# Performance work log

Measured on AMD Instinct MI355X. Metric: run time of the kernel, lower is better.

Reference implementation:

```python
import jax, jax.numpy as jnp
import numpy as np

B, S, D, H = 4, 2048, 1024, 16
HD = D // H

def rotate_half(x):
    x1, x2 = jnp.split(x, 2, axis=-1)
    return jnp.concatenate((-x2, x1), axis=-1)

def apply_rope(x, cos, sin):
    # x: [B,H,S,hd]; cos/sin: [S,hd] -> broadcast over B,H
    return x * cos[None, None] + rotate_half(x) * sin[None, None]

def setup_inputs() -> dict:
    key = jax.random.key(0)
    ks = jax.random.split(key, 8)
    x = jax.random.normal(ks[0], (B, S, D), dtype=jnp.float32)
    mask = jnp.triu(jnp.ones((S, S), dtype=bool), k=1)  # True = masked (causal)
    pos = jnp.arange(S, dtype=jnp.float32)[:, None]
    inv = 1.0 / (10000.0 ** (jnp.arange(0, HD, 2, dtype=jnp.float32) / HD))
    ang = pos * inv[None, :]  # [S, hd/2]
    ang = jnp.concatenate([ang, ang], axis=-1)  # [S, hd]
    rope_cos = jnp.cos(ang)
    rope_sin = jnp.sin(ang)
    scale = 1.0 / np.sqrt(D)
    Wq = jax.random.normal(ks[1], (D, D), dtype=jnp.float32) * scale
    Wk = jax.random.normal(ks[2], (D, D), dtype=jnp.float32) * scale
    Wv = jax.random.normal(ks[3], (D, D), dtype=jnp.float32) * scale
    Wo = jax.random.normal(ks[4], (D, D), dtype=jnp.float32) * scale
    z = jnp.zeros((D,), dtype=jnp.float32)
    return {"x": x, "mask": mask, "rope_cos": rope_cos, "rope_sin": rope_sin,
            "Wq": Wq, "bq": z, "Wk": Wk, "bk": z, "Wv": Wv, "bv": z, "Wo": Wo, "bo": z}

def reference(x, mask, rope_cos, rope_sin, Wq, bq, Wk, bk, Wv, bv, Wo, bo):
    b, s, d = x.shape
    def proj(W, bias):
        y = x @ W.T + bias  # torch Linear: x W^T + b
        return y.reshape(b, s, H, HD).transpose(0, 2, 1, 3)  # [B,H,S,hd]
    Q = apply_rope(proj(Wq, bq), rope_cos, rope_sin)
    K = apply_rope(proj(Wk, bk), rope_cos, rope_sin)
    V = proj(Wv, bv)
    scores = jnp.einsum('bhqd,bhkd->bhqk', Q, K) / jnp.sqrt(jnp.float32(HD))
    scores = jnp.where(mask[None, None], -jnp.inf, scores)
    attn = jax.nn.softmax(scores, axis=-1)
    ctx = jnp.einsum('bhqk,bhkd->bhqd', attn, V)
    ctx = ctx.transpose(0, 2, 1, 3).reshape(b, s, d)
    return ctx @ Wo.T + bo
```

## Files before the change

kernel.cpp:

```cpp
#include <hip/hip_runtime.h>
#include <hip/hip_bf16.h>

#define S_LEN 2048
#define D_MODEL 1024
#define NH 16
#define HDIM 64
#define B_SZ 4

typedef __attribute__((ext_vector_type(8))) short bf16x8;
typedef __attribute__((ext_vector_type(4))) float f32x4;

__device__ inline void gld16(const __hip_bfloat16* g, __hip_bfloat16* l) {
    __builtin_amdgcn_global_load_lds(
        (const __attribute__((address_space(1))) unsigned int*)g,
        (__attribute__((address_space(3))) unsigned int*)l, 16, 0, 0);
}

__device__ inline unsigned int pkbf(float a, float b) {
    float2 f; f.x = a; f.y = b;
    __hip_bfloat162 h = __float22bfloat162_rn(f);
    union { __hip_bfloat162 h; unsigned int u; } cv; cv.h = h; return cv.u;
}

__global__ __launch_bounds__(256) void f2bf4_kernel(const float4* __restrict__ in,
                                                    __hip_bfloat162* __restrict__ out,
                                                    int n4) {
    int i = blockIdx.x * 256 + threadIdx.x;
    if (i < n4) {
        float4 v = in[i];
        __hip_bfloat162 a, b;
        a.x = __float2bfloat16(v.x); a.y = __float2bfloat16(v.y);
        b.x = __float2bfloat16(v.z); b.y = __float2bfloat16(v.w);
        out[2 * i]     = a;
        out[2 * i + 1] = b;
    }
}

__global__ __launch_bounds__(256) void f2bfw_kernel(
    const float4* __restrict__ w0, const float4* __restrict__ w1,
    const float4* __restrict__ w2, const float4* __restrict__ w3,
    __hip_bfloat162* __restrict__ o0, __hip_bfloat162* __restrict__ o1,
    __hip_bfloat162* __restrict__ o2, __hip_bfloat162* __restrict__ o3) {
    const int z = blockIdx.y;
    const float4* in = (z == 0) ? w0 : (z == 1) ? w1 : (z == 2) ? w2 : w3;
    __hip_bfloat162* out = (z == 0) ? o0 : (z == 1) ? o1 : (z == 2) ? o2 : o3;
    int i = blockIdx.x * 256 + threadIdx.x;
    float4 v = in[i];
    __hip_bfloat162 a, b;
    a.x = __float2bfloat16(v.x); a.y = __float2bfloat16(v.y);
    b.x = __float2bfloat16(v.z); b.y = __float2bfloat16(v.w);
    out[2 * i]     = a;
    out[2 * i + 1] = b;
}

__device__ inline void gemm_mainloop(const __hip_bfloat16* __restrict__ X,
                                     const __hip_bfloat16* __restrict__ W,
                                     __hip_bfloat16* As, __hip_bfloat16* Bs,
                                     int m0, int n0, f32x4 acc[4][4]) {
    const int tid = threadIdx.x;
    const int wv = tid >> 6, lane = tid & 63, l15 = lane & 15, quad = lane >> 4;
    const int rw = (wv >> 1) * 64, cw = (wv & 1) * 64;
    const int r0 = tid >> 2, c0 = (tid & 3) * 8;
    const int r1 = (tid + 256) >> 2, c1 = ((tid + 256) & 3) * 8;
    const __hip_bfloat16* xa0 = &X[(size_t)(m0 + r0) * D_MODEL + c0];
    const __hip_bfloat16* xa1 = &X[(size_t)(m0 + r1) * D_MODEL + c1];
    const __hip_bfloat16* wa0 = &W[(size_t)(n0 + r0) * D_MODEL + c0];
    const __hip_bfloat16* wa1 = &W[(size_t)(n0 + r1) * D_MODEL + c1];
    const int la0 = r0 * 32 + c0, la1 = r1 * 32 + c1;

    gld16(xa0, &As[la0]); gld16(xa1, &As[la1]);
    gld16(wa0, &Bs[la0]); gld16(wa1, &Bs[la1]);
    __syncthreads();
    for (int k0 = 0; k0 < D_MODEL; k0 += 32) {
        const int buf = (k0 >> 5) & 1;
        if (k0 + 32 < D_MODEL) {
            const int o = (buf ^ 1) * 4096;
            gld16(xa0 + k0 + 32, &As[o + la0]);
            gld16(xa1 + k0 + 32, &As[o + la1]);
            gld16(wa0 + k0 + 32, &Bs[o + la0]);
            gld16(wa1 + k0 + 32, &Bs[o + la1]);
        }
        const __hip_bfloat16* Ab = &As[buf * 4096];
        const __hip_bfloat16* Bb = &Bs[buf * 4096];
        bf16x8 af[4], bfr[4];
#pragma unroll
        for (int t = 0; t < 4; t++)
            af[t] = *(const bf16x8*)&Ab[(rw + t * 16 + l15) * 32 + quad * 8];
#pragma unroll
        for (int t = 0; t < 4; t++)
            bfr[t] = *(const bf16x8*)&Bb[(cw + t * 16 + l15) * 32 + quad * 8];
#pragma unroll
        for (int mt = 0; mt < 4; mt++)
#pragma unroll
            for (int nt = 0; nt < 4; nt++)
                acc[mt][nt] = __builtin_amdgcn_mfma_f32_16x16x32_bf16(
                    af[mt], bfr[nt], acc[mt][nt], 0, 0, 0);
        __syncthreads();
    }
}

#define PT 136
__global__ __launch_bounds__(256) void qkv_kernel(
    const __hip_bfloat16* __restrict__ X,
    const __hip_bfloat16* __restrict__ W0, const __hip_bfloat16* __restrict__ W1,
    const __hip_bfloat16* __restrict__ W2,
    const float* __restrict__ b0, const float* __restrict__ b1,
    const float* __restrict__ b2,
    const float* __restrict__ rc, const float* __restrict__ rs,
    __hip_bfloat16* __restrict__ Qo, __hip_bfloat16* __restrict__ Ko,
    __hip_bfloat16* __restrict__ Vo) {
    __shared__ __hip_bfloat16 pool[16384];
    __hip_bfloat16* As = pool;
    __hip_bfloat16* Bs = pool + 8192;
    const int z = blockIdx.z;
    const __hip_bfloat16* W = (z == 0) ? W0 : ((z == 1) ? W1 : W2);
    const float* bias = (z == 0) ? b0 : ((z == 1) ? b1 : b2);
    f32x4 acc[4][4];
#pragma unroll
    for (int i = 0; i < 4; i++)
#pragma unroll
        for (int j = 0; j < 4; j++) acc[i][j] = (f32x4){0.f, 0.f, 0.f, 0.f};
    const int m0 = blockIdx.x * 128, n0 = blockIdx.y * 128;
    gemm_mainloop(X, W, As, Bs, m0, n0, acc);

    const int tid = threadIdx.x;
    const int wv = tid >> 6, lane = tid & 63, l15 = lane & 15, quad = lane >> 4;
    const int rw = (wv >> 1) * 64, cw = (wv & 1) * 64;

    if (z == 2) {
        __hip_bfloat16* T = pool;
        const int b = m0 >> 11, s0l = m0 & (S_LEN - 1);
#pragma unroll
        for (int hn = 0; hn < 2; hn++) {
            __syncthreads();
            if ((wv & 1) == hn) {
#pragma unroll
                for (int mt = 0; mt < 4; mt++)
#pragma unroll
                    for (int nt = 0; nt < 4; nt++)
#pragma unroll
                        for (int r = 0; r < 4; r++) {
                            int dl = nt * 16 + l15;
                            int ml = rw + mt * 16 + quad * 4 + r;
                            T[dl * PT + ml] =
                                __float2bfloat16(acc[mt][nt][r] + bias[n0 + hn * 64 + dl]);
                        }
            }
            __syncthreads();
            const int d = tid >> 2, sc = tid & 3;
            const int h = (n0 >> 6) + hn;
            size_t gb = ((size_t)((b * NH + h) * HDIM + d)) * S_LEN + s0l + sc * 32;
#pragma unroll
            for (int j = 0; j < 4; j++) {
                bf16x8 v = *(const bf16x8*)&T[d * PT + sc * 32 + j * 8];
                *(bf16x8*)&Vo[gb + j * 8] = v;
            }
        }
    } else {
        __hip_bfloat16* dst = (z == 0) ? Qo : Ko;
        const float qs = (z == 0) ? 0.18033688011112042f : 1.0f;
#pragma unroll
        for (int mt = 0; mt < 4; mt++)
#pragma unroll
            for (int r = 0; r < 4; r++) {
                int m = m0 + rw + mt * 16 + quad * 4 + r;
                int s = m & (S_LEN - 1), b = m >> 11;
#pragma unroll
                for (int nt = 0; nt < 2; nt++) {
                    int n1 = n0 + cw + nt * 16 + l15;
                    int h = n1 >> 6, hd1 = n1 & 63;
                    float y1 = acc[mt][nt][r] + bias[n1];
                    float y2 = acc[mt][nt + 2][r] + bias[n1 + 32];
                    float c1 = rc[s * HDIM + hd1], s1 = rs[s * HDIM + hd1];
                    float c2 = rc[s * HDIM + hd1 + 32], s2 = rs[s * HDIM + hd1 + 32];
                    size_t base = (((size_t)(b * NH + h)) * S_LEN + s) * HDIM;
                    dst[base + hd1]      = __float2bfloat16((y1 * c1 - y2 * s1) * qs);
                    dst[base + hd1 + 32] = __float2bfloat16((y2 * c2 + y1 * s2) * qs);
                }
            }
    }
}

#define SWZ(r, c) (((r) << 6) + ((c) ^ (((r) & 7) << 3)))
__global__ __launch_bounds__(256) void attn_kernel(
    const __hip_bfloat16* __restrict__ Q, const __hip_bfloat16* __restrict__ K,
    const __hip_bfloat16* __restrict__ VT, __hip_bfloat16* __restrict__ CTX) {
    __shared__ __hip_bfloat16 Kl[2][64 * 64];
    __shared__ __hip_bfloat16 Vl[2][64 * 64];
    __shared__ __hip_bfloat16 Pl[2][4][16 * 64];
    const int tid = threadIdx.x;
    const int wv = tid >> 6, lane = tid & 63, l15 = lane & 15, quad = lane >> 4;
    const int bh = blockIdx.x;
    const int pr = blockIdx.y;
    const int tA = pr, tC = 31 - pr;
    const int nkb = tC + 1;
    const size_t off = (size_t)bh * S_LEN * HDIM;
    const __hip_bfloat16* Qp = Q + off;
    const __hip_bfloat16* Kp = K + off;
    const __hip_bfloat16* Vp = VT + off;
    __hip_bfloat16* PC = &Pl[0][wv][0];
    __hip_bfloat16* PA = &Pl[1][wv][0];

    const int e0 = wv * 512 + lane * 8;
    const int r0 = e0 >> 6, c80 = e0 & 63;
    const int sw0 = c80 ^ ((r0 & 7) << 3);
    const int r1 = r0 + 32;
    const int sw1 = c80 ^ ((r1 & 7) << 3);
    const __hip_bfloat16* ks0 = Kp + r0 * 64 + sw0;
    const __hip_bfloat16* ks1 = Kp + r1 * 64 + sw1;
    const __hip_bfloat16* vs0 = Vp + (size_t)r0 * S_LEN + sw0;
    const __hip_bfloat16* vs1 = Vp + (size_t)r1 * S_LEN + sw1;

    auto stage = [&](int kb, int bsel) {
        const int ko = kb * 64;
        gld16(ks0 + (size_t)ko * 64, &Kl[bsel][e0]);
        gld16(ks1 + (size_t)ko * 64, &Kl[bsel][e0 + 2048]);
        gld16(vs0 + ko, &Vl[bsel][e0]);
        gld16(vs1 + ko, &Vl[bsel][e0 + 2048]);
    };

    bf16x8 qfA[2], qfC[2];
#pragma unroll
    for (int c = 0; c < 2; c++) {
        qfA[c] = *(const bf16x8*)&Qp[(size_t)(tA * 64 + wv * 16 + l15) * HDIM + c * 32 + quad * 8];
        qfC[c] = *(const bf16x8*)&Qp[(size_t)(tC * 64 + wv * 16 + l15) * HDIM + c * 32 + quad * 8];
    }

    float lA = 0.f, lC = 0.f;
    f32x4 accA[4], accC[4];
#pragma unroll
    for (int nt = 0; nt < 4; nt++) {
        accA[nt] = (f32x4){0.f, 0.f, 0.f, 0.f};
        accC[nt] = (f32x4){0.f, 0.f, 0.f, 0.f};
    }

    const int qrel = wv * 16 + l15;

    stage(0, 0);
    __syncthreads();
    for (int kb = 0; kb < nkb; kb++) {
        const int buf = kb & 1;
        if (kb + 1 < nkb) stage(kb + 1, buf ^ 1);
        const __hip_bfloat16* Kb_ = &Kl[buf][0];
        const __hip_bfloat16* Vb_ = &Vl[buf][0];

        const bool aAct = (kb <= tA);
        unsigned int pkC[8], pkA[8];

        f32x4 saC[4], saA[4];
#pragma unroll
        for (int st = 0; st < 4; st++) {
            saC[st] = (f32x4){0.f, 0.f, 0.f, 0.f};
            saA[st] = (f32x4){0.f, 0.f, 0.f, 0.f};
        }
        if (aAct) {
#pragma unroll
            for (int c = 0; c < 2; c++)
#pragma unroll
                for (int st = 0; st < 4; st++) {
                    bf16x8 kf = *(const bf16x8*)&Kb_[SWZ(st * 16 + l15, c * 32 + quad * 8)];
                    saC[st] = __builtin_amdgcn_mfma_f32_16x16x32_bf16(kf, qfC[c], saC[st], 0, 0, 0);
                    saA[st] = __builtin_amdgcn_mfma_f32_16x16x32_bf16(kf, qfA[c], saA[st], 0, 0, 0);
                }
        } else {
#pragma unroll
            for (int c = 0; c < 2; c++)
#pragma unroll
                for (int st = 0; st < 4; st++) {
                    bf16x8 kf = *(const bf16x8*)&Kb_[SWZ(st * 16 + l15, c * 32 + quad * 8)];
                    saC[st] = __builtin_amdgcn_mfma_f32_16x16x32_bf16(kf, qfC[c], saC[st], 0, 0, 0);
                }
        }

        {
            float ls = 0.f;
            if (kb == tC) {
#pragma unroll
                for (int st = 0; st < 4; st++) {
                    float p[4];
#pragma unroll
                    for (int r = 0; r < 4; r++) {
                        bool msk = (st * 16 + quad * 4 + r > qrel);
                        p[r] = msk ? 0.f : __builtin_exp2f(saC[st][r]);
                        ls += p[r];
                    }
                    pkC[st * 2 + 0] = pkbf(p[0], p[1]);
                    pkC[st * 2 + 1] = pkbf(p[2], p[3]);
                }
            } else {
#pragma unroll
                for (int st = 0; st < 4; st++) {
                    float p[4];
#pragma unroll
                    for (int r = 0; r < 4; r++) {
                        p[r] = __builtin_exp2f(saC[st][r]);
                        ls += p[r];
                    }
                    pkC[st * 2 + 0] = pkbf(p[0], p[1]);
                    pkC[st * 2 + 1] = pkbf(p[2], p[3]);
                }
            }
            ls += __shfl_xor(ls, 16);
            ls += __shfl_xor(ls, 32);
            lC += ls;
#pragma unroll
            for (int st = 0; st < 4; st++) {
                uint2 w; w.x = pkC[st * 2]; w.y = pkC[st * 2 + 1];
                *(uint2*)&PC[SWZ(l15, st * 16 + quad * 4)] = w;
            }
        }
        if (aAct) {
            float ls = 0.f;
            if (kb == tA) {
#pragma unroll
                for (int st = 0; st < 4; st++) {
                    float p[4];
#pragma unroll
                    for (int r = 0; r < 4; r++) {
                        bool msk = (st * 16 + quad * 4 + r > qrel);
                        p[r] = msk ? 0.f : __builtin_exp2f(saA[st][r]);
                        ls += p[r];
                    }
                    pkA[st * 2 + 0] = pkbf(p[0], p[1]);
                    pkA[st * 2 + 1] = pkbf(p[2], p[3]);
                }
            } else {
#pragma unroll
                for (int st = 0; st < 4; st++) {
                    float p[4];
#pragma unroll
                    for (int r = 0; r < 4; r++) {
                        p[r] = __builtin_exp2f(saA[st][r]);
                        ls += p[r];
                    }
                    pkA[st * 2 + 0] = pkbf(p[0], p[1]);
                    pkA[st * 2 + 1] = pkbf(p[2], p[3]);
                }
            }
            ls += __shfl_xor(ls, 16);
            ls += __shfl_xor(ls, 32);
            lA += ls;
#pragma unroll
            for (int st = 0; st < 4; st++) {
                uint2 w; w.x = pkA[st * 2]; w.y = pkA[st * 2 + 1];
                *(uint2*)&PA[SWZ(l15, st * 16 + quad * 4)] = w;
            }
        }

#pragma unroll
        for (int c = 0; c < 2; c++) {
            bf16x8 vf[4];
#pragma unroll
            for (int nt = 0; nt < 4; nt++)
                vf[nt] = *(const bf16x8*)&Vb_[SWZ(nt * 16 + l15, c * 32 + quad * 8)];
            {
                bf16x8 pf = *(const bf16x8*)&PC[SWZ(l15, c * 32 + quad * 8)];
#pragma unroll
                for (int nt = 0; nt < 4; nt++)
                    accC[nt] = __builtin_amdgcn_mfma_f32_16x16x32_bf16(vf[nt], pf, accC[nt], 0, 0, 0);
            }
            if (aAct) {
                bf16x8 pf = *(const bf16x8*)&PA[SWZ(l15, c * 32 + quad * 8)];
#pragma unroll
                for (int nt = 0; nt < 4; nt++)
                    accA[nt] = __builtin_amdgcn_mfma_f32_16x16x32_bf16(vf[nt], pf, accA[nt], 0, 0, 0);
            }
        }

        __syncthreads();
    }

    const int b = bh >> 4, h = bh & 15;
    {
        const int q = tA * 64 + wv * 16 + l15;
        const float inv = 1.0f / lA;
#pragma unroll
        for (int nt = 0; nt < 4; nt++) {
            uint2 st2;
            st2.x = pkbf(accA[nt][0] * inv, accA[nt][1] * inv);
            st2.y = pkbf(accA[nt][2] * inv, accA[nt][3] * inv);
            *(uint2*)&CTX[((size_t)(b * S_LEN + q)) * D_MODEL + h * HDIM + nt * 16 + quad * 4] = st2;
        }
    }
    {
        const int q = tC * 64 + wv * 16 + l15;
        const float inv = 1.0f / lC;
#pragma unroll
        for (int nt = 0; nt < 4; nt++) {
            uint2 st2;
            st2.x = pkbf(accC[nt][0] * inv, accC[nt][1] * inv);
            st2.y = pkbf(accC[nt][2] * inv, accC[nt][3] * inv);
            *(uint2*)&CTX[((size_t)(b * S_LEN + q)) * D_MODEL + h * HDIM + nt * 16 + quad * 4] = st2;
        }
    }
}

__global__ __launch_bounds__(256) void outproj_kernel(
    const __hip_bfloat16* __restrict__ X, const __hip_bfloat16* __restrict__ W,
    const float* __restrict__ bias, float* __restrict__ OUT) {
    __shared__ __hip_bfloat16 As[2 * 4096];
    __shared__ __hip_bfloat16 Bs[2 * 4096];
    f32x4 acc[4][4];
#pragma unroll
    for (int i = 0; i < 4; i++)
#pragma unroll
        for (int j = 0; j < 4; j++) acc[i][j] = (f32x4){0.f, 0.f, 0.f, 0.f};
    const int m0 = blockIdx.x * 128, n0 = blockIdx.y * 128;
    gemm_mainloop(X, W, As, Bs, m0, n0, acc);
    const int tid = threadIdx.x;
    const int wv = tid >> 6, lane = tid & 63, l15 = lane & 15, quad = lane >> 4;
    const int rw = (wv >> 1) * 64, cw = (wv & 1) * 64;
#pragma unroll
    for (int mt = 0; mt < 4; mt++)
#pragma unroll
        for (int r = 0; r < 4; r++) {
            int m = m0 + rw + mt * 16 + quad * 4 + r;
#pragma unroll
            for (int nt = 0; nt < 4; nt++) {
                int n = n0 + cw + nt * 16 + l15;
                OUT[(size_t)m * D_MODEL + n] = acc[mt][nt][r] + bias[n];
            }
        }
}

extern "C" void kernel_launch(void* const* d_in, const int* in_sizes, int n_in,
                              void* d_out, int out_size, void* d_ws, size_t ws_size,
                              hipStream_t stream) {
    const float* x  = (const float*)d_in[0];
    const float* rc = (const float*)d_in[2];
    const float* rs = (const float*)d_in[3];
    const float* Wq = (const float*)d_in[4];
    const float* bq = (const float*)d_in[5];
    const float* Wk = (const float*)d_in[6];
    const float* bk = (const float*)d_in[7];
    const float* Wv = (const float*)d_in[8];
    const float* bv = (const float*)d_in[9];
    const float* Wo = (const float*)d_in[10];
    const float* bo = (const float*)d_in[11];

    char* ws = (char*)d_ws;
    __hip_bfloat16* xbf = (__hip_bfloat16*)(ws);
    __hip_bfloat16* wqb = (__hip_bfloat16*)(ws + (16u << 20));
    __hip_bfloat16* wkb = (__hip_bfloat16*)(ws + (18u << 20));
    __hip_bfloat16* wvb = (__hip_bfloat16*)(ws + (20u << 20));
    __hip_bfloat16* wob = (__hip_bfloat16*)(ws + (22u << 20));
    __hip_bfloat16* Qb  = (__hip_bfloat16*)(ws + (24u << 20));
    __hip_bfloat16* Kb  = (__hip_bfloat16*)(ws + (40u << 20));
    __hip_bfloat16* Vb  = (__hip_bfloat16*)(ws + (56u << 20));
    __hip_bfloat16* Cb  = (__hip_bfloat16*)(ws + (72u << 20));
    float* out = (float*)d_out;

    f2bf4_kernel<<<8192, 256, 0, stream>>>((const float4*)x, (__hip_bfloat162*)xbf, 2097152);
    f2bfw_kernel<<<dim3(1024, 4), 256, 0, stream>>>(
        (const float4*)Wq, (const float4*)Wk, (const float4*)Wv, (const float4*)Wo,
        (__hip_bfloat162*)wqb, (__hip_bfloat162*)wkb, (__hip_bfloat162*)wvb,
        (__hip_bfloat162*)wob);

    qkv_kernel<<<dim3(64, 8, 3), 256, 0, stream>>>(xbf, wqb, wkb, wvb, bq, bk, bv,
                                                   rc, rs, Qb, Kb, Vb);
    attn_kernel<<<dim3(64, 16), 256, 0, stream>>>(Qb, Kb, Vb, Cb);
    outproj_kernel<<<dim3(64, 8), 256, 0, stream>>>(Cb, wob, bo, out);
}
```

Measured before the change: 302.6 us.

## Fuse Q and K projections in one block sharing the X tile

The QKV kernel now has two z-slices. One computes Q and K together, loading each X tile once and running MFMAs against both Wq and Wk tiles with two accumulator sets. The other computes V alone. This removes the redundant X loads for the K projection, at the cost of double the accumulator registers and more LDS per block, which may lower occupancy despite the launch_bounds hint. The load address setup is also simplified and the B-buffer stride is templated.

New measurement: 310.9 us. +2.7%, slower.

```diff
diff --git a/kernel.cpp b/kernel.cpp
--- a/kernel.cpp
+++ b/kernel.cpp
@@ -53,6 +53,7 @@
     out[2 * i + 1] = b;
 }
 
+template <int BSTRIDE>
 __device__ inline void gemm_mainloop(const __hip_bfloat16* __restrict__ X,
                                      const __hip_bfloat16* __restrict__ W,
                                      __hip_bfloat16* As, __hip_bfloat16* Bs,
@@ -61,12 +62,11 @@
     const int wv = tid >> 6, lane = tid & 63, l15 = lane & 15, quad = lane >> 4;
     const int rw = (wv >> 1) * 64, cw = (wv & 1) * 64;
     const int r0 = tid >> 2, c0 = (tid & 3) * 8;
-    const int r1 = (tid + 256) >> 2, c1 = ((tid + 256) & 3) * 8;
     const __hip_bfloat16* xa0 = &X[(size_t)(m0 + r0) * D_MODEL + c0];
-    const __hip_bfloat16* xa1 = &X[(size_t)(m0 + r1) * D_MODEL + c1];
+    const __hip_bfloat16* xa1 = xa0 + (size_t)64 * D_MODEL;
     const __hip_bfloat16* wa0 = &W[(size_t)(n0 + r0) * D_MODEL + c0];
-    const __hip_bfloat16* wa1 = &W[(size_t)(n0 + r1) * D_MODEL + c1];
-    const int la0 = r0 * 32 + c0, la1 = r1 * 32 + c1;
+    const __hip_bfloat16* wa1 = wa0 + (size_t)64 * D_MODEL;
+    const int la0 = r0 * 32 + c0, la1 = la0 + 2048;
 
     gld16(xa0, &As[la0]); gld16(xa1, &As[la1]);
     gld16(wa0, &Bs[la0]); gld16(wa1, &Bs[la1]);
@@ -74,14 +74,13 @@
     for (int k0 = 0; k0 < D_MODEL; k0 += 32) {
         const int buf = (k0 >> 5) & 1;
         if (k0 + 32 < D_MODEL) {
-            const int o = (buf ^ 1) * 4096;
-            gld16(xa0 + k0 + 32, &As[o + la0]);
-            gld16(xa1 + k0 + 32, &As[o + la1]);
-            gld16(wa0 + k0 + 32, &Bs[o + la0]);
-            gld16(wa1 + k0 + 32, &Bs[o + la1]);
+            gld16(xa0 + k0 + 32, &As[(buf ^ 1) * 4096 + la0]);
+            gld16(xa1 + k0 + 32, &As[(buf ^ 1) * 4096 + la1]);
+            gld16(wa0 + k0 + 32, &Bs[(buf ^ 1) * BSTRIDE + la0]);
+            gld16(wa1 + k0 + 32, &Bs[(buf ^ 1) * BSTRIDE + la1]);
         }
         const __hip_bfloat16* Ab = &As[buf * 4096];
-        const __hip_bfloat16* Bb = &Bs[buf * 4096];
+        const __hip_bfloat16* Bb = &Bs[buf * BSTRIDE];
         bf16x8 af[4], bfr[4];
 #pragma unroll
         for (int t = 0; t < 4; t++)
@@ -100,7 +99,7 @@
 }
 
 #define PT 136
-__global__ __launch_bounds__(256) void qkv_kernel(
+__global__ __launch_bounds__(256, 2) void qkv_kernel(
     const __hip_bfloat16* __restrict__ X,
     const __hip_bfloat16* __restrict__ W0, const __hip_bfloat16* __restrict__ W1,
     const __hip_bfloat16* __restrict__ W2,
@@ -109,26 +108,22 @@
     const float* __restrict__ rc, const float* __restrict__ rs,
     __hip_bfloat16* __restrict__ Qo, __hip_bfloat16* __restrict__ Ko,
     __hip_bfloat16* __restrict__ Vo) {
-    __shared__ __hip_bfloat16 pool[16384];
-    __hip_bfloat16* As = pool;
-    __hip_bfloat16* Bs = pool + 8192;
-    const int z = blockIdx.z;
-    const __hip_bfloat16* W = (z == 0) ? W0 : ((z == 1) ? W1 : W2);
-    const float* bias = (z == 0) ? b0 : ((z == 1) ? b1 : b2);
-    f32x4 acc[4][4];
-#pragma unroll
-    for (int i = 0; i < 4; i++)
-#pragma unroll
-        for (int j = 0; j < 4; j++) acc[i][j] = (f32x4){0.f, 0.f, 0.f, 0.f};
-    const int m0 = blockIdx.x * 128, n0 = blockIdx.y * 128;
-    gemm_mainloop(X, W, As, Bs, m0, n0, acc);
-
+    __shared__ __hip_bfloat16 As[2 * 4096];
+    __shared__ __hip_bfloat16 Bs[2 * 2 * 4096];
     const int tid = threadIdx.x;
     const int wv = tid >> 6, lane = tid & 63, l15 = lane & 15, quad = lane >> 4;
     const int rw = (wv >> 1) * 64, cw = (wv & 1) * 64;
-
-    if (z == 2) {
-        __hip_bfloat16* T = pool;
+    const int m0 = blockIdx.x * 128, n0 = blockIdx.y * 128;
+
+    if (blockIdx.z == 1) {
+        f32x4 acc[4][4];
+#pragma unroll
+        for (int i = 0; i < 4; i++)
+#pragma unroll
+            for (int j = 0; j < 4; j++) acc[i][j] = (f32x4){0.f, 0.f, 0.f, 0.f};
+        gemm_mainloop<8192>(X, W2, As, Bs, m0, n0, acc);
+
+        __hip_bfloat16* T = Bs;
         const int b = m0 >> 11, s0l = m0 & (S_LEN - 1);
 #pragma unroll
         for (int hn = 0; hn < 2; hn++) {
@@ -143,7 +138,7 @@
                             int dl = nt * 16 + l15;
                             int ml = rw + mt * 16 + quad * 4 + r;
                             T[dl * PT + ml] =
-                                __float2bfloat16(acc[mt][nt][r] + bias[n0 + hn * 64 + dl]);
+                                __float2bfloat16(acc[mt][nt][r] + b2[n0 + hn * 64 + dl]);
                         }
             }
             __syncthreads();
@@ -156,9 +151,73 @@
                 *(bf16x8*)&Vo[gb + j * 8] = v;
             }
         }
-    } else {
-        __hip_bfloat16* dst = (z == 0) ? Qo : Ko;
-        const float qs = (z == 0) ? 0.18033688011112042f : 1.0f;
+        return;
+    }
+
+    f32x4 acc0[4][4], acc1[4][4];
+#pragma unroll
+    for (int i = 0; i < 4; i++)
+#pragma unroll
+        for (int j = 0; j < 4; j++) {
+            acc0[i][j] = (f32x4){0.f, 0.f, 0.f, 0.f};
+            acc1[i][j] = (f32x4){0.f, 0.f, 0.f, 0.f};
+        }
+    {
+        const int r0 = tid >> 2, c0 = (tid & 3) * 8;
+        const __hip_bfloat16* xa0 = &X[(size_t)(m0 + r0) * D_MODEL + c0];
+        const __hip_bfloat16* xa1 = xa0 + (size_t)64 * D_MODEL;
+        const __hip_bfloat16* wq0 = &W0[(size_t)(n0 + r0) * D_MODEL + c0];
+        const __hip_bfloat16* wq1 = wq0 + (size_t)64 * D_MODEL;
+        const __hip_bfloat16* wk0 = &W1[(size_t)(n0 + r0) * D_MODEL + c0];
+        const __hip_bfloat16* wk1 = wk0 + (size_t)64 * D_MODEL;
+        const int la0 = r0 * 32 + c0, la1 = la0 + 2048;
+
+        gld16(xa0, &As[la0]);        gld16(xa1, &As[la1]);
+        gld16(wq0, &Bs[la0]);        gld16(wq1, &Bs[la1]);
+        gld16(wk0, &Bs[4096 + la0]); gld16(wk1, &Bs[4096 + la1]);
+        __syncthreads();
+        for (int k0 = 0; k0 < D_MODEL; k0 += 32) {
+            const int buf = (k0 >> 5) & 1;
+            if (k0 + 32 < D_MODEL) {
+                const int o = (buf ^ 1) * 4096, ob = (buf ^ 1) * 8192;
+                gld16(xa0 + k0 + 32, &As[o + la0]);
+                gld16(xa1 + k0 + 32, &As[o + la1]);
+                gld16(wq0 + k0 + 32, &Bs[ob + la0]);
+                gld16(wq1 + k0 + 32, &Bs[ob + la1]);
+                gld16(wk0 + k0 + 32, &Bs[ob + 4096 + la0]);
+                gld16(wk1 + k0 + 32, &Bs[ob + 4096 + la1]);
+            }
+            const __hip_bfloat16* Ab  = &As[buf * 4096];
+            const __hip_bfloat16* Bq  = &Bs[buf * 8192];
+            const __hip_bfloat16* Bk  = &Bs[buf * 8192 + 4096];
+            bf16x8 af[4], bq[4], bk[4];
+#pragma unroll
+            for (int t = 0; t < 4; t++)
+                af[t] = *(const bf16x8*)&Ab[(rw + t * 16 + l15) * 32 + quad * 8];
+#pragma unroll
+            for (int t = 0; t < 4; t++)
+                bq[t] = *(const bf16x8*)&Bq[(cw + t * 16 + l15) * 32 + quad * 8];
+#pragma unroll
+            for (int t = 0; t < 4; t++)
+                bk[t] = *(const bf16x8*)&Bk[(cw + t * 16 + l15) * 32 + quad * 8];
+#pragma unroll
+            for (int mt = 0; mt < 4; mt++)
+#pragma unroll
+                for (int nt = 0; nt < 4; nt++)
+                    acc0[mt][nt] = __builtin_amdgcn_mfma_f32_16x16x32_bf16(
+                        af[mt], bq[nt], acc0[mt][nt], 0, 0, 0);
+#pragma unroll
+            for (int mt = 0; mt < 4; mt++)
+#pragma unroll
+                for (int nt = 0; nt < 4; nt++)
+                    acc1[mt][nt] = __builtin_amdgcn_mfma_f32_16x16x32_bf16(
+                        af[mt], bk[nt], acc1[mt][nt], 0, 0, 0);
+            __syncthreads();
+        }
+    }
+
+    {
+        const float qs = 0.18033688011112042f;
 #pragma unroll
         for (int mt = 0; mt < 4; mt++)
 #pragma unroll
@@ -169,13 +228,34 @@
                 for (int nt = 0; nt < 2; nt++) {
                     int n1 = n0 + cw + nt * 16 + l15;
                     int h = n1 >> 6, hd1 = n1 & 63;
-                    float y1 = acc[mt][nt][r] + bias[n1];
-                    float y2 = acc[mt][nt + 2][r] + bias[n1 + 32];
+                    float y1 = acc0[mt][nt][r] + b0[n1];
+                    float y2 = acc0[mt][nt + 2][r] + b0[n1 + 32];
                     float c1 = rc[s * HDIM + hd1], s1 = rs[s * HDIM + hd1];
                     float c2 = rc[s * HDIM + hd1 + 32], s2 = rs[s * HDIM + hd1 + 32];
                     size_t base = (((size_t)(b * NH + h)) * S_LEN + s) * HDIM;
-                    dst[base + hd1]      = __float2bfloat16((y1 * c1 - y2 * s1) * qs);
-                    dst[base + hd1 + 32] = __float2bfloat16((y2 * c2 + y1 * s2) * qs);
+                    Qo[base + hd1]      = __float2bfloat16((y1 * c1 - y2 * s1) * qs);
+                    Qo[base + hd1 + 32] = __float2bfloat16((y2 * c2 + y1 * s2) * qs);
+                }
+            }
+    }
+    {
+#pragma unroll
+        for (int mt = 0; mt < 4; mt++)
+#pragma unroll
+            for (int r = 0; r < 4; r++) {
+                int m = m0 + rw + mt * 16 + quad * 4 + r;
+                int s = m & (S_LEN - 1), b = m >> 11;
+#pragma unroll
+                for (int nt = 0; nt < 2; nt++) {
+                    int n1 = n0 + cw + nt * 16 + l15;
+                    int h = n1 >> 6, hd1 = n1 & 63;
+                    float y1 = acc1[mt][nt][r] + b1[n1];
+                    float y2 = acc1[mt][nt + 2][r] + b1[n1 + 32];
+                    float c1 = rc[s * HDIM + hd1], s1 = rs[s * HDIM + hd1];
+                    float c2 = rc[s * HDIM + hd1 + 32], s2 = rs[s * HDIM + hd1 + 32];
+                    size_t base = (((size_t)(b * NH + h)) * S_LEN + s) * HDIM;
+                    Ko[base + hd1]      = __float2bfloat16(y1 * c1 - y2 * s1);
+                    Ko[base + hd1 + 32] = __float2bfloat16(y2 * c2 + y1 * s2);
                 }
             }
     }
@@ -406,7 +486,7 @@
 #pragma unroll
         for (int j = 0; j < 4; j++) acc[i][j] = (f32x4){0.f, 0.f, 0.f, 0.f};
     const int m0 = blockIdx.x * 128, n0 = blockIdx.y * 128;
-    gemm_mainloop(X, W, As, Bs, m0, n0, acc);
+    gemm_mainloop<4096>(X, W, As, Bs, m0, n0, acc);
     const int tid = threadIdx.x;
     const int wv = tid >> 6, lane = tid & 63, l15 = lane & 15, quad = lane >> 4;
     const int rw = (wv >> 1) * 64, cw = (wv & 1) * 64;
@@ -456,7 +536,7 @@
         (__hip_bfloat162*)wqb, (__hip_bfloat162*)wkb, (__hip_bfloat162*)wvb,
         (__hip_bfloat162*)wob);
 
-    qkv_kernel<<<dim3(64, 8, 3), 256, 0, stream>>>(xbf, wqb, wkb, wvb, bq, bk, bv,
+    qkv_kernel<<<dim3(64, 8, 2), 256, 0, stream>>>(xbf, wqb, wkb, wvb, bq, bk, bv,
                                                    rc, rs, Qb, Kb, Vb);
     attn_kernel<<<dim3(64, 16), 256, 0, stream>>>(Qb, Kb, Vb, Cb);
     outproj_kernel<<<dim3(64, 8), 256, 0, stream>>>(Cb, wob, bo, out);
```

## Use 256x256 tiles with 512 threads and swizzled LDS for QKV GEMM

Applied to the files above, without the earlier changes.

Replaces the 128x128, 256-thread QKV projection GEMM with a 256x256 tile computed by 8 waves, each holding an 8x4 MFMA accumulator block. K steps grow to 64 and the LDS staging uses an XOR swizzle to avoid bank conflicts. The aim is more operand reuse per loaded byte and fewer global loads. The trade-off is far fewer blocks (384 instead of 1536), which may underfill the GPU's CUs, plus higher register and LDS use per block.

New measurement: 328.2 us. 1.08x slower.

```diff
diff --git a/kernel.cpp b/kernel.cpp
--- a/kernel.cpp
+++ b/kernel.cpp
@@ -53,6 +53,143 @@
     out[2 * i + 1] = b;
 }
 
+__device__ inline void gemm256_mainloop(const __hip_bfloat16* __restrict__ X,
+                                        const __hip_bfloat16* __restrict__ W,
+                                        __hip_bfloat16* As, __hip_bfloat16* Bs,
+                                        int m0, int n0, f32x4 acc[8][4]) {
+    const int tid = threadIdx.x;
+    const int wv = tid >> 6, lane = tid & 63, l15 = lane & 15, quad = lane >> 4;
+    const int wr = wv >> 2, wc = wv & 3;
+    const int row_s = tid >> 3;
+    const int csw = ((tid & 7) ^ (row_s & 7)) * 8;
+    const __hip_bfloat16* xsrc = X + (size_t)(m0 + row_s) * D_MODEL + csw;
+    const __hip_bfloat16* wsrc = W + (size_t)(n0 + row_s) * D_MODEL + csw;
+    const int ld = tid * 8;
+
+    auto stage = [&](int k0, int bsel) {
+#pragma unroll
+        for (int i = 0; i < 4; i++) {
+            gld16(xsrc + (size_t)(i * 64) * D_MODEL + k0,
+                  &As[bsel * 16384 + i * 4096 + ld]);
+            gld16(wsrc + (size_t)(i * 64) * D_MODEL + k0,
+                  &Bs[bsel * 16384 + i * 4096 + ld]);
+        }
+    };
+
+    stage(0, 0);
+    __syncthreads();
+    for (int kt = 0; kt < 16; kt++) {
+        const int buf = kt & 1;
+        if (kt + 1 < 16) stage((kt + 1) * 64, buf ^ 1);
+        const __hip_bfloat16* Ab = &As[buf * 16384];
+        const __hip_bfloat16* Bb = &Bs[buf * 16384];
+#pragma unroll
+        for (int kc = 0; kc < 2; kc++) {
+            bf16x8 af[8], bfr[4];
+#pragma unroll
+            for (int mt = 0; mt < 8; mt++) {
+                int row = wr * 128 + mt * 16 + l15;
+                af[mt] = *(const bf16x8*)&Ab[row * 64 + (((kc * 4 + quad) ^ (l15 & 7)) * 8)];
+            }
+#pragma unroll
+            for (int nt = 0; nt < 4; nt++) {
+                int row = wc * 64 + nt * 16 + l15;
+                bfr[nt] = *(const bf16x8*)&Bb[row * 64 + (((kc * 4 + quad) ^ (l15 & 7)) * 8)];
+            }
+#pragma unroll
+            for (int mt = 0; mt < 8; mt++)
+#pragma unroll
+                for (int nt = 0; nt < 4; nt++)
+                    acc[mt][nt] = __builtin_amdgcn_mfma_f32_16x16x32_bf16(
+                        af[mt], bfr[nt], acc[mt][nt], 0, 0, 0);
+        }
+        __syncthreads();
+    }
+}
+
+#define PT 264
+__global__ __launch_bounds__(512, 2) void qkv_kernel(
+    const __hip_bfloat16* __restrict__ X,
+    const __hip_bfloat16* __restrict__ W0, const __hip_bfloat16* __restrict__ W1,
+    const __hip_bfloat16* __restrict__ W2,
+    const float* __restrict__ b0, const float* __restrict__ b1,
+    const float* __restrict__ b2,
+    const float* __restrict__ rc, const float* __restrict__ rs,
+    __hip_bfloat16* __restrict__ Qo, __hip_bfloat16* __restrict__ Ko,
+    __hip_bfloat16* __restrict__ Vo) {
+    __shared__ __hip_bfloat16 As[2 * 16384];
+    __shared__ __hip_bfloat16 Bs[2 * 16384];
+    const int z = blockIdx.z;
+    const __hip_bfloat16* W = (z == 0) ? W0 : ((z == 1) ? W1 : W2);
+    f32x4 acc[8][4];
+#pragma unroll
+    for (int i = 0; i < 8; i++)
+#pragma unroll
+        for (int j = 0; j < 4; j++) acc[i][j] = (f32x4){0.f, 0.f, 0.f, 0.f};
+    const int m0 = blockIdx.x * 256, n0 = blockIdx.y * 256;
+    gemm256_mainloop(X, W, As, Bs, m0, n0, acc);
+
+    const int tid = threadIdx.x;
+    const int wv = tid >> 6, lane = tid & 63, l15 = lane & 15, quad = lane >> 4;
+    const int wr = wv >> 2, wc = wv & 3;
+
+    if (z == 2) {
+        __hip_bfloat16* T = As;
+        const int b = m0 >> 11, s0l = m0 & (S_LEN - 1);
+#pragma unroll
+        for (int hn = 0; hn < 4; hn++) {
+            __syncthreads();
+            if (wc == hn) {
+#pragma unroll
+                for (int mt = 0; mt < 8; mt++)
+#pragma unroll
+                    for (int nt = 0; nt < 4; nt++)
+#pragma unroll
+                        for (int r = 0; r < 4; r++) {
+                            int dl = nt * 16 + l15;
+                            int ml = wr * 128 + mt * 16 + quad * 4 + r;
+                            T[dl * PT + ml] =
+                                __float2bfloat16(acc[mt][nt][r] + b2[n0 + hn * 64 + dl]);
+                        }
+            }
+            __syncthreads();
+            const int d = tid >> 3, sc = tid & 7;
+            const int h = (n0 >> 6) + hn;
+            size_t gb = ((size_t)((b * NH + h) * HDIM + d)) * S_LEN + s0l + sc * 32;
+#pragma unroll
+            for (int j = 0; j < 4; j++) {
+                bf16x8 v = *(const bf16x8*)&T[d * PT + sc * 32 + j * 8];
+                *(bf16x8*)&Vo[gb + j * 8] = v;
+            }
+        }
+        return;
+    }
+
+    __hip_bfloat16* dst = (z == 0) ? Qo : Ko;
+    const float* bias = (z == 0) ? b0 : b1;
+    const float qs = (z == 0) ? 0.18033688011112042f : 1.0f;
+#pragma unroll
+    for (int mt = 0; mt < 8; mt++)
+#pragma unroll
+        for (int r = 0; r < 4; r++) {
+            int m = m0 + wr * 128 + mt * 16 + quad * 4 + r;
+            int s = m & (S_LEN - 1), b = m >> 11;
+#pragma unroll
+            for (int nt = 0; nt < 2; nt++) {
+                int hd1 = nt * 16 + l15;
+                int n1 = n0 + wc * 64 + hd1;
+                int h = n1 >> 6;
+                float y1 = acc[mt][nt][r] + bias[n1];
+                float y2 = acc[mt][nt + 2][r] + bias[n1 + 32];
+                float c1 = rc[s * HDIM + hd1], s1 = rs[s * HDIM + hd1];
+                float c2 = rc[s * HDIM + hd1 + 32], s2 = rs[s * HDIM + hd1 + 32];
+                size_t base = (((size_t)(b * NH + h)) * S_LEN + s) * HDIM;
+                dst[base + hd1]      = __float2bfloat16((y1 * c1 - y2 * s1) * qs);
+                dst[base + hd1 + 32] = __float2bfloat16((y2 * c2 + y1 * s2) * qs);
+            }
+        }
+}
+
 __device__ inline void gemm_mainloop(const __hip_bfloat16* __restrict__ X,
                                      const __hip_bfloat16* __restrict__ W,
                                      __hip_bfloat16* As, __hip_bfloat16* Bs,
@@ -96,88 +233,6 @@
                 acc[mt][nt] = __builtin_amdgcn_mfma_f32_16x16x32_bf16(
                     af[mt], bfr[nt], acc[mt][nt], 0, 0, 0);
         __syncthreads();
-    }
-}
-
-#define PT 136
-__global__ __launch_bounds__(256) void qkv_kernel(
-    const __hip_bfloat16* __restrict__ X,
-    const __hip_bfloat16* __restrict__ W0, const __hip_bfloat16* __restrict__ W1,
-    const __hip_bfloat16* __restrict__ W2,
-    const float* __restrict__ b0, const float* __restrict__ b1,
-    const float* __restrict__ b2,
-    const float* __restrict__ rc, const float* __restrict__ rs,
-    __hip_bfloat16* __restrict__ Qo, __hip_bfloat16* __restrict__ Ko,
-    __hip_bfloat16* __restrict__ Vo) {
-    __shared__ __hip_bfloat16 pool[16384];
-    __hip_bfloat16* As = pool;
-    __hip_bfloat16* Bs = pool + 8192;
-    const int z = blockIdx.z;
-    const __hip_bfloat16* W = (z == 0) ? W0 : ((z == 1) ? W1 : W2);
-    const float* bias = (z == 0) ? b0 : ((z == 1) ? b1 : b2);
-    f32x4 acc[4][4];
-#pragma unroll
-    for (int i = 0; i < 4; i++)
-#pragma unroll
-        for (int j = 0; j < 4; j++) acc[i][j] = (f32x4){0.f, 0.f, 0.f, 0.f};
-    const int m0 = blockIdx.x * 128, n0 = blockIdx.y * 128;
-    gemm_mainloop(X, W, As, Bs, m0, n0, acc);
-
-    const int tid = threadIdx.x;
-    const int wv = tid >> 6, lane = tid & 63, l15 = lane & 15, quad = lane >> 4;
-    const int rw = (wv >> 1) * 64, cw = (wv & 1) * 64;
-
-    if (z == 2) {
-        __hip_bfloat16* T = pool;
-        const int b = m0 >> 11, s0l = m0 & (S_LEN - 1);
-#pragma unroll
-        for (int hn = 0; hn < 2; hn++) {
-            __syncthreads();
-            if ((wv & 1) == hn) {
-#pragma unroll
-                for (int mt = 0; mt < 4; mt++)
-#pragma unroll
-                    for (int nt = 0; nt < 4; nt++)
-#pragma unroll
-                        for (int r = 0; r < 4; r++) {
-                            int dl = nt * 16 + l15;
-                            int ml = rw + mt * 16 + quad * 4 + r;
-                            T[dl * PT + ml] =
-                                __float2bfloat16(acc[mt][nt][r] + bias[n0 + hn * 64 + dl]);
-                        }
-            }
-            __syncthreads();
-            const int d = tid >> 2, sc = tid & 3;
-            const int h = (n0 >> 6) + hn;
-            size_t gb = ((size_t)((b * NH + h) * HDIM + d)) * S_LEN + s0l + sc * 32;
-#pragma unroll
-            for (int j = 0; j < 4; j++) {
-                bf16x8 v = *(const bf16x8*)&T[d * PT + sc * 32 + j * 8];
-                *(bf16x8*)&Vo[gb + j * 8] = v;
-            }
-        }
-    } else {
-        __hip_bfloat16* dst = (z == 0) ? Qo : Ko;
-        const float qs = (z == 0) ? 0.18033688011112042f : 1.0f;
-#pragma unroll
-        for (int mt = 0; mt < 4; mt++)
-#pragma unroll
-            for (int r = 0; r < 4; r++) {
-                int m = m0 + rw + mt * 16 + quad * 4 + r;
-                int s = m & (S_LEN - 1), b = m >> 11;
-#pragma unroll
-                for (int nt = 0; nt < 2; nt++) {
-                    int n1 = n0 + cw + nt * 16 + l15;
-                    int h = n1 >> 6, hd1 = n1 & 63;
-                    float y1 = acc[mt][nt][r] + bias[n1];
-                    float y2 = acc[mt][nt + 2][r] + bias[n1 + 32];
-                    float c1 = rc[s * HDIM + hd1], s1 = rs[s * HDIM + hd1];
-                    float c2 = rc[s * HDIM + hd1 + 32], s2 = rs[s * HDIM + hd1 + 32];
-                    size_t base = (((size_t)(b * NH + h)) * S_LEN + s) * HDIM;
-                    dst[base + hd1]      = __float2bfloat16((y1 * c1 - y2 * s1) * qs);
-                    dst[base + hd1 + 32] = __float2bfloat16((y2 * c2 + y1 * s2) * qs);
-                }
-            }
     }
 }
 
@@ -456,7 +511,7 @@
         (__hip_bfloat162*)wqb, (__hip_bfloat162*)wkb, (__hip_bfloat162*)wvb,
         (__hip_bfloat162*)wob);
 
-    qkv_kernel<<<dim3(64, 8, 3), 256, 0, stream>>>(xbf, wqb, wkb, wvb, bq, bk, bv,
+    qkv_kernel<<<dim3(32, 4, 3), 512, 0, stream>>>(xbf, wqb, wkb, wvb, bq, bk, bv,
                                                    rc, rs, Qb, Kb, Vb);
     attn_kernel<<<dim3(64, 16), 256, 0, stream>>>(Qb, Kb, Vb, Cb);
     outproj_kernel<<<dim3(64, 8), 256, 0, stream>>>(Cb, wob, bo, out);
```
